# Kernel optimization log

Measured on AMD Instinct MI355X. Metric: run time of the kernel, lower is better.

The kernel has to match this reference:

```python
import jax, jax.numpy as jnp
import numpy as np

T, B, M = 512, 64, 512
DM = 384  # memory_size
DX = 384  # input_size
H = 192   # hidden_size
A = 192   # attention_size


def setup_inputs() -> dict:
    key = jax.random.key(0)
    ks = iter(jax.random.split(key, 24))

    def rn(shape, s):
        return jax.random.normal(next(ks), shape, jnp.float32) * s

    inp = {
        "memory": rn((M, B, DM), 1.0),
        "memory_mask": jnp.ones((M, B), jnp.bool_),
        "input": rn((T, B, DX), 1.0),
    }
    for suf in ("fw", "bw"):
        inp[f"Wm_{suf}"] = rn((DM, A), 0.08)
        inp[f"Wx_{suf}"] = rn((DX, A), 0.08)
        inp[f"Wh_{suf}"] = rn((H, A), 0.08)
        inp[f"v_{suf}"] = rn((A,), 0.08)
        inp[f"Wg_{suf}"] = rn((DX + DM, DX + DM), 0.05)
        inp[f"Wih_{suf}"] = rn((DX + DM, 3 * H), 0.05)
        inp[f"Whh_{suf}"] = rn((H, 3 * H), 0.08)
        inp[f"bih_{suf}"] = jnp.zeros((3 * H,), jnp.float32)
        inp[f"bhh_{suf}"] = jnp.zeros((3 * H,), jnp.float32)
    return inp


def _direction(x, memory, mask, Wm, Wx, Wh, v, Wg, Wih, Whh, bih, bhh):
    """Unroll one gated-attention GRU direction. x:[T,B,DX], memory:[M,B,DM]."""
    mem_proj = jnp.einsum('mbd,da->mba', memory, Wm)  # [M,B,A], hoisted out of scan
    x_proj = jnp.einsum('tbd,da->tba', x, Wx)         # [T,B,A]
    h0 = jnp.zeros((x.shape[1], Whh.shape[0]), x.dtype)
    neg = jnp.asarray(-1e9, x.dtype)

    def step(h, xs):
        x_t, xp_t = xs
        # additive attention over memory positions
        s = jnp.einsum('mba,a->mb', jnp.tanh(mem_proj + xp_t[None] + (h @ Wh)[None]), v)
        s = jnp.where(mask, s, neg)
        a = jax.nn.softmax(s, axis=0)                 # softmax over M
        c = jnp.einsum('mb,mbd->bd', a, memory)       # context [B,DM]
        xc = jnp.concatenate([x_t, c], axis=-1)       # [B,DX+DM]
        xc = jax.nn.sigmoid(xc @ Wg) * xc             # R-net input gate
        gi = xc @ Wih + bih
        gh = h @ Whh + bhh
        ir, iz, inn = jnp.split(gi, 3, axis=-1)
        hr, hz, hn = jnp.split(gh, 3, axis=-1)
        r = jax.nn.sigmoid(ir + hr)
        z = jax.nn.sigmoid(iz + hz)
        n = jnp.tanh(inn + r * hn)
        h_new = (1 - z) * n + z * h                   # torch GRUCell update
        return h_new, h_new

    _, ys = jax.lax.scan(step, h0, (x, x_proj))
    return ys  # [T,B,H]


def reference(memory, memory_mask, input,
              Wm_fw, Wx_fw, Wh_fw, v_fw, Wg_fw, Wih_fw, Whh_fw, bih_fw, bhh_fw,
              Wm_bw, Wx_bw, Wh_bw, v_bw, Wg_bw, Wih_bw, Whh_bw, bih_bw, bhh_bw):
    out_fw = _direction(input, memory, memory_mask,
                        Wm_fw, Wx_fw, Wh_fw, v_fw, Wg_fw, Wih_fw, Whh_fw, bih_fw, bhh_fw)
    out_bw = _direction(input[::-1], memory, memory_mask,
                        Wm_bw, Wx_bw, Wh_bw, v_bw, Wg_bw, Wih_bw, Whh_bw, bih_bw, bhh_bw)[::-1]
    # dropout is identity in eval mode
    return jnp.concatenate([out_fw, out_bw], axis=-1)  # [T,B,2H]
```

## Files before the change

### kernel.cpp

```cpp
#include <hip/hip_runtime.h>
#include <hip/hip_fp16.h>

#define TT 512
#define MM 512
#define NWG 256

__device__ __forceinline__ float fast_sigmoid(float x) {
  float e = __expf(-x);
  return __builtin_amdgcn_rcpf(1.f + e);
}
__device__ __forceinline__ float fast_tanh(float x) {
  float e = __expf(2.f * x);
  return 1.f - 2.f * __builtin_amdgcn_rcpf(e + 1.f);
}
__device__ __forceinline__ float2 h2f2(unsigned u) {
  __half2 h = *reinterpret_cast<__half2*>(&u);
  return __half22float2(h);
}
__device__ __forceinline__ unsigned pack2(float x, float y) {
  __half2 h = __floats2half2_rn(x, y);
  return *reinterpret_cast<unsigned*>(&h);
}

typedef _Float16 hf2_t __attribute__((ext_vector_type(2)));
__device__ __forceinline__ float fdot2f(unsigned a, unsigned b, float c) {
#if __has_builtin(__builtin_amdgcn_fdot2)
  union U { unsigned u; hf2_t h; };
  U ua, ub; ua.u = a; ub.u = b;
  return __builtin_amdgcn_fdot2(ua.h, ub.h, c, false);
#else
  float2 fa = h2f2(a), fb = h2f2(b);
  return fmaf(fa.x, fb.x, fmaf(fa.y, fb.y, c));
#endif
}

template<int K, int S>
__device__ __forceinline__ float dotpipe(const unsigned* __restrict__ w,
                                         const unsigned* __restrict__ x2) {
  unsigned A[12], B[12];
  float acc[4] = {0.f, 0.f, 0.f, 0.f};
  #pragma unroll
  for (int i = 0; i < 12; ++i) A[i] = w[(size_t)i * S];
  #pragma unroll 1
  for (int k = 0; k < K; k += 24) {
    #pragma unroll
    for (int i = 0; i < 12; ++i) B[i] = w[(size_t)(k + 12 + i) * S];
    #pragma unroll
    for (int i = 0; i < 12; ++i) acc[i & 3] = fdot2f(A[i], x2[k + i], acc[i & 3]);
    if (k + 24 < K) {
      #pragma unroll
      for (int i = 0; i < 12; ++i) A[i] = w[(size_t)(k + 24 + i) * S];
    }
    #pragma unroll
    for (int i = 0; i < 12; ++i) acc[i & 3] = fdot2f(B[i], x2[k + 12 + i], acc[i & 3]);
  }
  return (acc[0] + acc[1]) + (acc[2] + acc[3]);
}

__device__ __forceinline__ void ast(float* p, float v) {
  __hip_atomic_store(p, v, __ATOMIC_RELAXED, __HIP_MEMORY_SCOPE_AGENT);
}
__device__ __forceinline__ float ald(const float* p) {
  return __hip_atomic_load(p, __ATOMIC_RELAXED, __HIP_MEMORY_SCOPE_AGENT);
}
__device__ __forceinline__ void astu(unsigned* p, unsigned v) {
  __hip_atomic_store(p, v, __ATOMIC_RELAXED, __HIP_MEMORY_SCOPE_AGENT);
}
__device__ __forceinline__ unsigned aldu(const unsigned* p) {
  return __hip_atomic_load(p, __ATOMIC_RELAXED, __HIP_MEMORY_SCOPE_AGENT);
}
__device__ __forceinline__ void astull(unsigned long long* p, unsigned long long v) {
  __hip_atomic_store(p, v, __ATOMIC_RELAXED, __HIP_MEMORY_SCOPE_AGENT);
}
__device__ __forceinline__ unsigned long long aldull(const unsigned long long* p) {
  return __hip_atomic_load(p, __ATOMIC_RELAXED, __HIP_MEMORY_SCOPE_AGENT);
}
union F2U { unsigned long long u; float f[2]; };

struct ProjParams {
  const float* X[4]; const float* W[4]; __half* C[4]; int rev[4]; int transp[4];
};

__global__ __launch_bounds__(192) void proj_kernel(ProjParams pp) {
  __shared__ float xs[32 * 384];
  const int job = blockIdx.y;
  const float* __restrict__ X = pp.X[job];
  const float* __restrict__ W = pp.W[job];
  __half* __restrict__ C = pp.C[job];
  const int rev = pp.rev[job];
  const int transp = pp.transp[job];
  const int r0 = blockIdx.x * 32;
  const int tid = threadIdx.x;

  for (int idx = tid; idx < 32 * 384; idx += 192) {
    int r = idx / 384, k = idx - r * 384;
    int row = r0 + r;
    int srow = row;
    if (rev) { int t = row >> 6, b2 = row & 63; srow = ((TT - 1 - t) << 6) | b2; }
    xs[idx] = X[(size_t)srow * 384 + k];
  }
  __syncthreads();

  float acc[32];
  #pragma unroll
  for (int r = 0; r < 32; ++r) acc[r] = 0.f;
  for (int k = 0; k < 384; ++k) {
    float w = W[k * 192 + tid];
    #pragma unroll
    for (int r = 0; r < 32; ++r) acc[r] = fmaf(xs[r * 384 + k], w, acc[r]);
  }
  #pragma unroll
  for (int r = 0; r < 32; ++r) {
    int row = r0 + r;
    size_t di = transp ? (((size_t)(row & 63) * MM + (row >> 6)) * 192 + tid)
                       : ((size_t)row * 192 + tid);
    C[di] = __float2half(acc[r]);
  }
}

__global__ __launch_bounds__(384) void memcvt_kernel(const float* __restrict__ src,
                                                     __half* __restrict__ dst) {
  int m = blockIdx.x, b = blockIdx.y, d = threadIdx.x;
  dst[((size_t)b * MM + m) * 384 + d] = __float2half(src[((size_t)m * 64 + b) * 384 + d]);
}

struct WcvtParams { const float* src[8]; unsigned* dst[8]; int tot[8]; int N[8]; };
__global__ __launch_bounds__(256) void wcvt_kernel(WcvtParams wp) {
  int job = blockIdx.y;
  const float* __restrict__ s = wp.src[job];
  unsigned* __restrict__ d = wp.dst[job];
  int n = wp.N[job], tot = wp.tot[job];
  for (int i = blockIdx.x * 256 + threadIdx.x; i < tot; i += gridDim.x * 256) {
    int k2 = i / n, j = i - k2 * n;
    d[i] = pack2(s[(size_t)(2 * k2) * n + j], s[(size_t)(2 * k2 + 1) * n + j]);
  }
}

#define L_MP     0
#define L_REDP   98304
#define L_SH384  110592
#define L_Q      112128
#define L_XCF    112896
#define L_XC2    115968
#define L_G2     117504
#define L_GIS    119040
#define L_GHS    120192
#define L_HF     121344
#define L_H2     122112
#define L_VS     122496
#define L_BIH    123264
#define L_BHH    124416
#define L_ZP     125568
#define L_MISC   125600
#define L_ES     125632
#define SCAN_LDS 126656
static_assert(SCAN_LDS <= 160 * 1024, "LDS overflow");

struct ScanParams {
  const float* input;
  const unsigned* memt;
  const unsigned* mpt[2];
  const __half* xp[2];
  const unsigned* Wh2[2];
  const unsigned* Wg2[2];
  const unsigned* Wih2[2];
  const unsigned* Whh2[2];
  const float* v[2];
  const float* bih[2];
  const float* bhh[2];
  unsigned long long* ectx;
  float* ez;
  unsigned* gmail;
  unsigned* hmail;
  unsigned* flags;
  float* out;
};

__global__ __launch_bounds__(512, 1) void scan_kernel(ScanParams p) {
  extern __shared__ char smem[];
  __half*   mp_s   = (__half*)(smem + L_MP);
  float*    redp   = (float*)(smem + L_REDP);
  float*    sh384  = (float*)(smem + L_SH384);
  float*    q_s    = (float*)(smem + L_Q);
  float*    xc_f   = (float*)(smem + L_XCF);
  unsigned* xc2_s  = (unsigned*)(smem + L_XC2);
  unsigned* g2_s   = (unsigned*)(smem + L_G2);
  float*    gis    = (float*)(smem + L_GIS);
  float*    ghs    = (float*)(smem + L_GHS);
  float*    h_f    = (float*)(smem + L_HF);
  unsigned* h2_s   = (unsigned*)(smem + L_H2);
  float*    v_s    = (float*)(smem + L_VS);
  float*    bih_s  = (float*)(smem + L_BIH);
  float*    bhh_s  = (float*)(smem + L_BHH);
  float*    zp_s   = (float*)(smem + L_ZP);
  float*    misc_s = (float*)(smem + L_MISC);
  float*    e_s    = (float*)(smem + L_ES);

  const int g = blockIdx.x;
  const int xcd = g & 7;
  const int slot = g >> 3;
  const int dir = xcd >> 2;
  const int idx = (xcd & 3) * 32 + slot;
  const int b = idx & 63;
  const int half = idx >> 6;
  const int tid = threadIdx.x;
  const int lane = tid & 63;
  const int wv = tid >> 6;

  const unsigned* __restrict__ Wh2  = p.Wh2[dir];
  const unsigned* __restrict__ Wg2  = p.Wg2[dir];
  const unsigned* __restrict__ Wih2 = p.Wih2[dir];
  const unsigned* __restrict__ Whh2 = p.Whh2[dir];
  const __half* __restrict__ xp = p.xp[dir];
  const int m0 = half * 256;

  const int idx_my = (dir * 2 + half) * 64 + b;
  const int idx_p  = (dir * 2 + (half ^ 1)) * 64 + b;
  unsigned long long* myctx_u = p.ectx + (size_t)idx_my * 2 * 192;
  const unsigned long long* pctx_u = p.ectx + (size_t)idx_p * 2 * 192;
  float* myz0 = p.ez + (size_t)idx_my * 2;
  const float* pz0 = p.ez + (size_t)idx_p * 2;
  unsigned* gmail_my = p.gmail + (size_t)idx_my * 2 * 192;
  const unsigned* gmail_p = p.gmail + (size_t)idx_p * 2 * 192;
  unsigned* hmail_my = p.hmail + (size_t)idx_my * 2 * 48;
  const unsigned* hmail_p = p.hmail + (size_t)idx_p * 2 * 48;
  unsigned* fctx_my = p.flags + idx_my;        const unsigned* fctx_p = p.flags + idx_p;
  unsigned* fg_my   = p.flags + 256 + idx_my;  const unsigned* fg_p   = p.flags + 256 + idx_p;
  unsigned* fh_my   = p.flags + 512 + idx_my;  const unsigned* fh_p   = p.flags + 512 + idx_p;

  {
    const unsigned* mpu = p.mpt[dir] + ((size_t)b * MM + m0) * 96;
    unsigned* mpd = (unsigned*)mp_s;
    for (int i = tid; i < 256 * 96; i += 512) mpd[i] = mpu[i];
    if (tid < 192) { h_f[tid] = 0.f; v_s[tid] = p.v[dir][tid]; }
    if (tid < 96) h2_s[tid] = 0u;
    if (tid < 288) {
      int c3 = tid / 96, jj = tid - c3 * 96;
      int col = c3 * 192 + 96 * half + jj;
      bih_s[tid] = p.bih[dir][col];
      bhh_s[tid] = p.bhh[dir][col];
    }
  }
  __syncthreads();
  const float v0 = v_s[lane], v1 = v_s[lane + 64], v2 = v_s[lane + 128];

  #pragma unroll 1
  for (int t = 0; t < TT; ++t) {
    const int par = t & 1;
    if (tid < 384) {
      const int kh = (tid >= 192);
      const int a = tid - 192 * kh;
      sh384[tid] = dotpipe<48, 192>(Wh2 + (size_t)kh * 48 * 192 + a, h2_s + kh * 48);
    }
    __syncthreads();
    if (tid < 192)
      q_s[tid] = __half2float(xp[((size_t)t * 64 + b) * 192 + tid]) + sh384[tid] + sh384[192 + tid];
    __syncthreads();

    {
      const float q0 = q_s[lane], q1 = q_s[lane + 64], q2 = q_s[lane + 128];
      float zacc = 0.f;
      const __half* mph = mp_s + (wv * 32) * 192;
      #pragma unroll 4
      for (int i = 0; i < 32; ++i) {
        const __half* r = mph + i * 192;
        float s = v0 * fast_tanh(__half2float(r[lane]) + q0)
                + v1 * fast_tanh(__half2float(r[lane + 64]) + q1)
                + v2 * fast_tanh(__half2float(r[lane + 128]) + q2);
        #pragma unroll
        for (int off = 32; off > 0; off >>= 1) s += __shfl_xor(s, off, 64);
        float e = __expf(s);
        zacc += e;
        if (lane == 0) e_s[wv * 32 + i] = e;
      }
      if (lane == 0) zp_s[wv] = zacc;
    }
    __syncthreads();
    {
      float ca[8] = {0, 0, 0, 0, 0, 0, 0, 0};
      if (lane < 48) {
        const uint4* mrow4 = (const uint4*)(p.memt + ((size_t)b * MM + m0 + wv * 32) * 192) + lane;
        const float* es = e_s + wv * 32;
        #pragma unroll 8
        for (int i = 0; i < 32; ++i) {
          uint4 mv = mrow4[(size_t)i * 48];
          float e = es[i];
          float2 f0 = h2f2(mv.x), f1 = h2f2(mv.y), f2 = h2f2(mv.z), f3 = h2f2(mv.w);
          ca[0] = fmaf(e, f0.x, ca[0]); ca[1] = fmaf(e, f0.y, ca[1]);
          ca[2] = fmaf(e, f1.x, ca[2]); ca[3] = fmaf(e, f1.y, ca[3]);
          ca[4] = fmaf(e, f2.x, ca[4]); ca[5] = fmaf(e, f2.y, ca[5]);
          ca[6] = fmaf(e, f3.x, ca[6]); ca[7] = fmaf(e, f3.y, ca[7]);
        }
        float2* rp2 = (float2*)(redp + wv * 384 + 8 * lane);
        rp2[0] = make_float2(ca[0], ca[1]);
        rp2[1] = make_float2(ca[2], ca[3]);
        rp2[2] = make_float2(ca[4], ca[5]);
        rp2[3] = make_float2(ca[6], ca[7]);
      }
    }
    __syncthreads();

    float zs = 0.f;
    if (tid < 192) {
      float cm0 = 0.f, cm1 = 0.f;
      const float2* rp2 = (const float2*)redp;
      #pragma unroll
      for (int k = 0; k < 8; ++k) {
        float2 v2r = rp2[k * 192 + tid];
        cm0 += v2r.x; cm1 += v2r.y;
      }
      sh384[2 * tid] = cm0; sh384[2 * tid + 1] = cm1;
      F2U u; u.f[0] = cm0; u.f[1] = cm1;
      astull(myctx_u + par * 192 + tid, u.u);
    }
    if (tid == 0) {
      #pragma unroll
      for (int k = 0; k < 8; ++k) zs += zp_s[k];
      ast(myz0 + par, zs);
    }
    const int xt = dir ? (TT - 1 - t) : t;
    if (tid < 384) xc_f[tid] = p.input[((size_t)xt * 64 + b) * 384 + tid];
    __syncthreads();
    if (tid < 192) xc2_s[tid] = pack2(xc_f[2 * tid], xc_f[2 * tid + 1]);
    if (tid == 0) astu(fctx_my, (unsigned)(t + 1));
    __syncthreads();

    float eacc = 0.f;
    if (tid < 384) {
      const int col = 384 * half + tid;
      eacc = dotpipe<192, 768>(Wg2 + col, xc2_s);
    }
    if (tid >= 384) {
      for (int jj = tid - 384; jj < 288; jj += 128) {
        const int c3 = jj / 96;
        const int col = c3 * 192 + 96 * half + (jj - c3 * 96);
        ghs[jj] = dotpipe<96, 576>(Whh2 + col, h2_s) + bhh_s[jj];
      }
    }
    if (tid == 0) {
      while (aldu(fctx_p) < (unsigned)(t + 1)) __builtin_amdgcn_s_sleep(1);
      float pz = ald(pz0 + par);
      misc_s[0] = __builtin_amdgcn_rcpf(zs + pz);
    }
    __syncthreads();

    if (tid < 192) {
      F2U u; u.u = aldull(pctx_u + par * 192 + tid);
      float iz = misc_s[0];
      float x0 = (sh384[2 * tid] + u.f[0]) * iz;
      float x1 = (sh384[2 * tid + 1] + u.f[1]) * iz;
      xc_f[384 + 2 * tid] = x0;
      xc_f[384 + 2 * tid + 1] = x1;
      xc2_s[192 + tid] = pack2(x0, x1);
    }
    __syncthreads();

    if (tid < 384) {
      const int col = 384 * half + tid;
      eacc += dotpipe<192, 768>(Wg2 + (size_t)192 * 768 + col, xc2_s + 192);
      sh384[tid] = fast_sigmoid(eacc) * xc_f[col];
    }
    __syncthreads();
    if (tid < 192) {
      unsigned pk = pack2(sh384[2 * tid], sh384[2 * tid + 1]);
      g2_s[192 * half + tid] = pk;
      astu(gmail_my + par * 192 + tid, pk);
    }
    __syncthreads();
    if (tid == 0) astu(fg_my, (unsigned)(t + 1));

    float gacc = 0.f;
    if (tid < 288) {
      const int c3 = tid / 96, jj = tid - c3 * 96;
      const int col = c3 * 192 + 96 * half + jj;
      gacc = dotpipe<192, 576>(Wih2 + (size_t)(192 * half) * 576 + col, g2_s + 192 * half);
    }
    if (tid == 0) {
      while (aldu(fg_p) < (unsigned)(t + 1)) __builtin_amdgcn_s_sleep(1);
    }
    __syncthreads();
    if (tid < 192) g2_s[192 * (1 - half) + tid] = aldu(gmail_p + par * 192 + tid);
    __syncthreads();

    if (tid < 288) {
      const int c3 = tid / 96, jj = tid - c3 * 96;
      const int col = c3 * 192 + 96 * half + jj;
      gis[tid] = gacc + bih_s[tid]
               + dotpipe<192, 576>(Wih2 + (size_t)(192 * (1 - half)) * 576 + col,
                                   g2_s + 192 * (1 - half));
    }
    __syncthreads();

    if (tid < 96) {
      const int j = 96 * half + tid;
      float r = fast_sigmoid(gis[tid] + ghs[tid]);
      float z = fast_sigmoid(gis[96 + tid] + ghs[96 + tid]);
      float n = fast_tanh(gis[192 + tid] + r * ghs[192 + tid]);
      float hnew = (1.f - z) * n + z * h_f[j];
      h_f[j] = hnew;
      int trow = dir ? (TT - 1 - t) : t;
      p.out[((size_t)trow * 64 + b) * 384 + dir * 192 + j] = hnew;
    }
    __syncthreads();
    if (tid < 48) {
      unsigned pk = pack2(h_f[96 * half + 2 * tid], h_f[96 * half + 2 * tid + 1]);
      h2_s[48 * half + tid] = pk;
      astu(hmail_my + par * 48 + tid, pk);
    }
    __syncthreads();
    if (tid == 0) {
      astu(fh_my, (unsigned)(t + 1));
      while (aldu(fh_p) < (unsigned)(t + 1)) __builtin_amdgcn_s_sleep(1);
    }
    __syncthreads();
    if (tid < 48) h2_s[48 * (1 - half) + tid] = aldu(hmail_p + par * 48 + tid);
    __syncthreads();
  }
}

extern "C" void kernel_launch(void* const* d_in, const int* in_sizes, int n_in,
                              void* d_out, int out_size, void* d_ws, size_t ws_size,
                              hipStream_t stream) {
  (void)in_sizes; (void)n_in; (void)out_size;
  const float* memory = (const float*)d_in[0];
  const float* input  = (const float*)d_in[2];
  const float* Wm[2]  = {(const float*)d_in[3],  (const float*)d_in[12]};
  const float* Wx[2]  = {(const float*)d_in[4],  (const float*)d_in[13]};
  const float* Wh[2]  = {(const float*)d_in[5],  (const float*)d_in[14]};
  const float* v[2]   = {(const float*)d_in[6],  (const float*)d_in[15]};
  const float* Wg[2]  = {(const float*)d_in[7],  (const float*)d_in[16]};
  const float* Wih[2] = {(const float*)d_in[8],  (const float*)d_in[17]};
  const float* Whh[2] = {(const float*)d_in[9],  (const float*)d_in[18]};
  const float* bih[2] = {(const float*)d_in[10], (const float*)d_in[19]};
  const float* bhh[2] = {(const float*)d_in[11], (const float*)d_in[20]};

  char* ws = (char*)d_ws;
  const size_t OFF_FLAGS = 0;
  const size_t OFF_EZ    = 4096;
  const size_t OFF_GMAIL = 6144;
  const size_t OFF_HMAIL = 792576;
  const size_t OFF_ECTX  = 989184;
  const size_t OFF_MPT0  = 1775616;
  const size_t OFF_MPT1  = OFF_MPT0 + 12582912;
  const size_t OFF_XP0   = OFF_MPT1 + 12582912;
  const size_t OFF_XP1   = OFF_XP0 + 12582912;
  const size_t OFF_MT    = OFF_XP1 + 12582912;
  const size_t OFF_WG0   = OFF_MT + 25165824;
  const size_t OFF_WG1   = OFF_WG0 + 1179648;
  const size_t OFF_WIH0  = OFF_WG1 + 1179648;
  const size_t OFF_WIH1  = OFF_WIH0 + 884736;
  const size_t OFF_WHH0  = OFF_WIH1 + 884736;
  const size_t OFF_WHH1  = OFF_WHH0 + 221184;
  const size_t OFF_WH0   = OFF_WHH1 + 221184;
  const size_t OFF_WH1   = OFF_WH0 + 73728;
  const size_t NEEDED    = OFF_WH1 + 73728;
  if (ws_size < NEEDED) return;

  unsigned* flags = (unsigned*)(ws + OFF_FLAGS);
  float* ez    = (float*)(ws + OFF_EZ);
  unsigned* gmail = (unsigned*)(ws + OFF_GMAIL);
  unsigned* hmail = (unsigned*)(ws + OFF_HMAIL);
  unsigned long long* ectx = (unsigned long long*)(ws + OFF_ECTX);
  __half* mpt0 = (__half*)(ws + OFF_MPT0);
  __half* mpt1 = (__half*)(ws + OFF_MPT1);
  __half* xp0  = (__half*)(ws + OFF_XP0);
  __half* xp1  = (__half*)(ws + OFF_XP1);
  __half* memt = (__half*)(ws + OFF_MT);
  unsigned* wg2[2]  = {(unsigned*)(ws + OFF_WG0),  (unsigned*)(ws + OFF_WG1)};
  unsigned* wih2[2] = {(unsigned*)(ws + OFF_WIH0), (unsigned*)(ws + OFF_WIH1)};
  unsigned* whh2[2] = {(unsigned*)(ws + OFF_WHH0), (unsigned*)(ws + OFF_WHH1)};
  unsigned* wh2[2]  = {(unsigned*)(ws + OFF_WH0),  (unsigned*)(ws + OFF_WH1)};

  hipFuncSetAttribute(reinterpret_cast<const void*>(scan_kernel),
                      hipFuncAttributeMaxDynamicSharedMemorySize, SCAN_LDS);

  hipMemsetAsync(ws + OFF_FLAGS, 0, 4096, stream);

  ProjParams pp;
  pp.X[0] = memory; pp.W[0] = Wm[0]; pp.C[0] = mpt0; pp.rev[0] = 0; pp.transp[0] = 1;
  pp.X[1] = memory; pp.W[1] = Wm[1]; pp.C[1] = mpt1; pp.rev[1] = 0; pp.transp[1] = 1;
  pp.X[2] = input;  pp.W[2] = Wx[0]; pp.C[2] = xp0;  pp.rev[2] = 0; pp.transp[2] = 0;
  pp.X[3] = input;  pp.W[3] = Wx[1]; pp.C[3] = xp1;  pp.rev[3] = 1; pp.transp[3] = 0;
  proj_kernel<<<dim3(1024, 4), dim3(192), 0, stream>>>(pp);
  memcvt_kernel<<<dim3(MM, 64), dim3(384), 0, stream>>>(memory, memt);

  WcvtParams wp;
  for (int d = 0; d < 2; ++d) {
    wp.src[d]     = Wg[d];  wp.dst[d]     = wg2[d];  wp.tot[d]     = 384 * 768; wp.N[d]     = 768;
    wp.src[2 + d] = Wih[d]; wp.dst[2 + d] = wih2[d]; wp.tot[2 + d] = 384 * 576; wp.N[2 + d] = 576;
    wp.src[4 + d] = Whh[d]; wp.dst[4 + d] = whh2[d]; wp.tot[4 + d] = 96 * 576;  wp.N[4 + d] = 576;
    wp.src[6 + d] = Wh[d];  wp.dst[6 + d] = wh2[d];  wp.tot[6 + d] = 96 * 192;  wp.N[6 + d] = 192;
  }
  wcvt_kernel<<<dim3(288, 8), dim3(256), 0, stream>>>(wp);

  ScanParams sp;
  sp.input = input;
  sp.memt = (const unsigned*)memt;
  sp.mpt[0] = (const unsigned*)mpt0; sp.mpt[1] = (const unsigned*)mpt1;
  sp.xp[0] = xp0; sp.xp[1] = xp1;
  for (int d = 0; d < 2; ++d) {
    sp.Wh2[d] = wh2[d]; sp.Wg2[d] = wg2[d]; sp.Wih2[d] = wih2[d]; sp.Whh2[d] = whh2[d];
    sp.v[d] = v[d]; sp.bih[d] = bih[d]; sp.bhh[d] = bhh[d];
  }
  sp.ectx = ectx; sp.ez = ez; sp.gmail = gmail; sp.hmail = hmail; sp.flags = flags;
  sp.out = (float*)d_out;
  scan_kernel<<<dim3(NWG), dim3(512), SCAN_LDS, stream>>>(sp);
}
```

Baseline: 22.44 ms.

## Remove per-step barriers by having consumer threads spin on partner flags directly

Several __syncthreads barriers per timestep are removed. The threads that consume partner data (context, gate mailbox, hidden mailbox) now each poll the cross-workgroup flag themselves instead of thread 0 polling and then a block barrier. The input row load is fused into the context-reduction threads as a float2 read with direct packing. The GRU cell update is merged with the hidden-state packing so each thread handles two elements. The goal is to shorten the serial per-step latency of the recurrence. The cost is more threads spinning on global flags and redundant z-sum computation.

```diff
diff --git a/kernel.cpp b/kernel.cpp
--- a/kernel.cpp
+++ b/kernel.cpp
@@ -193,7 +193,6 @@
   float*    bih_s  = (float*)(smem + L_BIH);
   float*    bhh_s  = (float*)(smem + L_BHH);
   float*    zp_s   = (float*)(smem + L_ZP);
-  float*    misc_s = (float*)(smem + L_MISC);
   float*    e_s    = (float*)(smem + L_ES);
 
   const int g = blockIdx.x;
@@ -300,7 +299,8 @@
     }
     __syncthreads();
 
-    float zs = 0.f;
+    const int xt = dir ? (TT - 1 - t) : t;
+    const float* xrow = p.input + ((size_t)xt * 64 + b) * 384;
     if (tid < 192) {
       float cm0 = 0.f, cm1 = 0.f;
       const float2* rp2 = (const float2*)redp;
@@ -312,41 +312,37 @@
       sh384[2 * tid] = cm0; sh384[2 * tid + 1] = cm1;
       F2U u; u.f[0] = cm0; u.f[1] = cm1;
       astull(myctx_u + par * 192 + tid, u.u);
+      float2 xi = ((const float2*)xrow)[tid];
+      xc_f[2 * tid] = xi.x; xc_f[2 * tid + 1] = xi.y;
+      xc2_s[tid] = pack2(xi.x, xi.y);
     }
     if (tid == 0) {
+      float zs = 0.f;
       #pragma unroll
       for (int k = 0; k < 8; ++k) zs += zp_s[k];
       ast(myz0 + par, zs);
     }
-    const int xt = dir ? (TT - 1 - t) : t;
-    if (tid < 384) xc_f[tid] = p.input[((size_t)xt * 64 + b) * 384 + tid];
-    __syncthreads();
-    if (tid < 192) xc2_s[tid] = pack2(xc_f[2 * tid], xc_f[2 * tid + 1]);
+    __syncthreads();
     if (tid == 0) astu(fctx_my, (unsigned)(t + 1));
-    __syncthreads();
 
     float eacc = 0.f;
     if (tid < 384) {
       const int col = 384 * half + tid;
       eacc = dotpipe<192, 768>(Wg2 + col, xc2_s);
-    }
-    if (tid >= 384) {
+    } else {
       for (int jj = tid - 384; jj < 288; jj += 128) {
         const int c3 = jj / 96;
         const int col = c3 * 192 + 96 * half + (jj - c3 * 96);
         ghs[jj] = dotpipe<96, 576>(Whh2 + col, h2_s) + bhh_s[jj];
       }
     }
-    if (tid == 0) {
+    if (tid < 192) {
       while (aldu(fctx_p) < (unsigned)(t + 1)) __builtin_amdgcn_s_sleep(1);
+      F2U u; u.u = aldull(pctx_u + par * 192 + tid);
+      float zl = ((zp_s[0] + zp_s[1]) + (zp_s[2] + zp_s[3]))
+               + ((zp_s[4] + zp_s[5]) + (zp_s[6] + zp_s[7]));
       float pz = ald(pz0 + par);
-      misc_s[0] = __builtin_amdgcn_rcpf(zs + pz);
-    }
-    __syncthreads();
-
-    if (tid < 192) {
-      F2U u; u.u = aldull(pctx_u + par * 192 + tid);
-      float iz = misc_s[0];
+      float iz = __builtin_amdgcn_rcpf(zl + pz);
       float x0 = (sh384[2 * tid] + u.f[0]) * iz;
       float x1 = (sh384[2 * tid + 1] + u.f[1]) * iz;
       xc_f[384 + 2 * tid] = x0;
@@ -361,6 +357,7 @@
       sh384[tid] = fast_sigmoid(eacc) * xc_f[col];
     }
     __syncthreads();
+
     if (tid < 192) {
       unsigned pk = pack2(sh384[2 * tid], sh384[2 * tid + 1]);
       g2_s[192 * half + tid] = pk;
@@ -375,11 +372,10 @@
       const int col = c3 * 192 + 96 * half + jj;
       gacc = dotpipe<192, 576>(Wih2 + (size_t)(192 * half) * 576 + col, g2_s + 192 * half);
     }
-    if (tid == 0) {
+    if (tid < 192) {
       while (aldu(fg_p) < (unsigned)(t + 1)) __builtin_amdgcn_s_sleep(1);
-    }
-    __syncthreads();
-    if (tid < 192) g2_s[192 * (1 - half) + tid] = aldu(gmail_p + par * 192 + tid);
+      g2_s[192 * (1 - half) + tid] = aldu(gmail_p + par * 192 + tid);
+    }
     __syncthreads();
 
     if (tid < 288) {
@@ -391,29 +387,30 @@
     }
     __syncthreads();
 
-    if (tid < 96) {
-      const int j = 96 * half + tid;
-      float r = fast_sigmoid(gis[tid] + ghs[tid]);
-      float z = fast_sigmoid(gis[96 + tid] + ghs[96 + tid]);
-      float n = fast_tanh(gis[192 + tid] + r * ghs[192 + tid]);
-      float hnew = (1.f - z) * n + z * h_f[j];
-      h_f[j] = hnew;
+    if (tid < 48) {
+      const int j0 = 96 * half + 2 * tid;
+      float r0 = fast_sigmoid(gis[2 * tid]       + ghs[2 * tid]);
+      float z0 = fast_sigmoid(gis[96 + 2 * tid]  + ghs[96 + 2 * tid]);
+      float n0 = fast_tanh(gis[192 + 2 * tid] + r0 * ghs[192 + 2 * tid]);
+      float hn0 = (1.f - z0) * n0 + z0 * h_f[j0];
+      float r1 = fast_sigmoid(gis[2 * tid + 1]      + ghs[2 * tid + 1]);
+      float z1 = fast_sigmoid(gis[96 + 2 * tid + 1] + ghs[96 + 2 * tid + 1]);
+      float n1 = fast_tanh(gis[192 + 2 * tid + 1] + r1 * ghs[192 + 2 * tid + 1]);
+      float hn1 = (1.f - z1) * n1 + z1 * h_f[j0 + 1];
+      h_f[j0] = hn0; h_f[j0 + 1] = hn1;
       int trow = dir ? (TT - 1 - t) : t;
-      p.out[((size_t)trow * 64 + b) * 384 + dir * 192 + j] = hnew;
-    }
-    __syncthreads();
-    if (tid < 48) {
-      unsigned pk = pack2(h_f[96 * half + 2 * tid], h_f[96 * half + 2 * tid + 1]);
+      float2* orow = (float2*)(p.out + ((size_t)trow * 64 + b) * 384 + dir * 192);
+      orow[48 * half + tid] = make_float2(hn0, hn1);
+      unsigned pk = pack2(hn0, hn1);
       h2_s[48 * half + tid] = pk;
       astu(hmail_my + par * 48 + tid, pk);
     }
     __syncthreads();
-    if (tid == 0) {
-      astu(fh_my, (unsigned)(t + 1));
+    if (tid == 0) astu(fh_my, (unsigned)(t + 1));
+    if (tid < 48) {
       while (aldu(fh_p) < (unsigned)(t + 1)) __builtin_amdgcn_s_sleep(1);
-    }
-    __syncthreads();
-    if (tid < 48) h2_s[48 * (1 - half) + tid] = aldu(hmail_p + par * 48 + tid);
+      h2_s[48 * (1 - half) + tid] = aldu(hmail_p + par * 48 + tid);
+    }
     __syncthreads();
   }
 }
```

Measured after the change: 22.29 ms. About the same (-0.6%).
